# Performance work log

Measured on AMD Instinct MI355X. Metric: run time of the kernel, lower is better.

The kernel has to match this reference:

```python
import jax, jax.numpy as jnp
from jax import lax
import numpy as np

B, L, E, H, R, V = 64, 512, 256, 256, 50, 20000
NEG = 1e10  # seq_max_pool mask constant


def _conv1d(x, w, b):
    # x: (B, L, Cin) -> (B, L, Cout); kernel 3, 'same' padding (pad=1)
    y = lax.conv_general_dilated(x.transpose(0, 2, 1), w, (1,), [(1, 1)],
                                 dimension_numbers=('NCH', 'OIH', 'NCH'))
    return y.transpose(0, 2, 1) + b


def _lstm_step(x, h, c, W_ih, W_hh, b_ih, b_hh):
    # single-step LSTM, PyTorch gate order (i, f, g, o)
    gates = x @ W_ih.T + b_ih + h @ W_hh.T + b_hh
    i, f, g, o = jnp.split(gates, 4, axis=-1)
    c = jax.nn.sigmoid(f) * c + jax.nn.sigmoid(i) * jnp.tanh(g)
    h = jax.nn.sigmoid(o) * jnp.tanh(c)
    return h, c


def _attention(q, ctx, W_attn, b_attn):
    # Luong attention (IBM seq2seq style). q: (B,E), ctx: (B,L,E)
    scores = jnp.einsum('be,ble->bl', q, ctx)
    attn = jax.nn.softmax(scores, axis=-1)
    mix = jnp.einsum('bl,ble->be', attn, ctx)
    return jnp.tanh(jnp.concatenate([mix, q], axis=-1) @ W_attn.T + b_attn)


def setup_inputs() -> dict:
    key = jax.random.key(0)
    ks = jax.random.split(key, 25)
    s = 0.05
    return {
        'encoder_o': jax.random.normal(ks[0], (B, L, E), jnp.float32),
        'h0': jax.random.normal(ks[1], (B, H), jnp.float32),
        'c0': jax.random.normal(ks[2], (B, H), jnp.float32),
        'sos_emb': jax.random.normal(ks[3], (E,), jnp.float32) * s,
        'rel_emb': jax.random.normal(ks[4], (R, E), jnp.float32) * s,
        'W_ih': jax.random.normal(ks[5], (4 * H, E), jnp.float32) * s,
        'W_hh': jax.random.normal(ks[6], (4 * H, H), jnp.float32) * s,
        'b_ih': jax.random.normal(ks[7], (4 * H,), jnp.float32) * s,
        'b_hh': jax.random.normal(ks[8], (4 * H,), jnp.float32) * s,
        'W_attn': jax.random.normal(ks[9], (E, 2 * E), jnp.float32) * s,
        'b_attn': jax.random.normal(ks[10], (E,), jnp.float32) * s,
        'conv_rel_w': jax.random.normal(ks[11], (E, 2 * H, 3), jnp.float32) * s,
        'conv_rel_b': jax.random.normal(ks[12], (E,), jnp.float32) * s,
        'conv_ent_w': jax.random.normal(ks[13], (E, 2 * H, 3), jnp.float32) * s,
        'conv_ent_b': jax.random.normal(ks[14], (E,), jnp.float32) * s,
        'W_rel': jax.random.normal(ks[15], (R, E), jnp.float32) * s,
        'b_rel': jax.random.normal(ks[16], (R,), jnp.float32) * s,
        'w_e1': jax.random.normal(ks[17], (E,), jnp.float32) * s,
        'b_e1': jax.random.normal(ks[18], (1,), jnp.float32) * s,
        'w_e2': jax.random.normal(ks[19], (E,), jnp.float32) * s,
        'b_e2': jax.random.normal(ks[20], (1,), jnp.float32) * s,
        'T': jax.random.randint(ks[21], (B, L), 0, V),
        'R_in': jax.random.randint(ks[22], (B,), 0, R),
        'S_K1': jax.random.randint(ks[23], (B,), 0, L),
        'S_K2': jax.random.randint(ks[24], (B,), 0, L),
    }


def reference(encoder_o, h0, c0, sos_emb, rel_emb, W_ih, W_hh, b_ih, b_hh,
              W_attn, b_attn, conv_rel_w, conv_rel_b, conv_ent_w, conv_ent_b,
              W_rel, b_rel, w_e1, b_e1, w_e2, b_e2, T, R_in, S_K1, S_K2):
    # train_forward, order=('subject','predicate','object') -> sos2ent, ent2rel, rel2ent
    # dropout is identity (eval mode)
    mask = (T > 0).astype(encoder_o.dtype)[..., None]  # (B,L,1)
    bidx = jnp.arange(B)

    def step(inp, h, c, enc, conv_w, conv_b):
        # forward_step: one LSTM step + attention over enc
        h, c = _lstm_step(inp, h, c, W_ih, W_hh, b_ih, b_hh)
        out = _attention(h, enc, W_attn, b_attn)  # (B,E)
        # seq_and_vec + permute + conv1d + permute
        cat = jnp.concatenate([enc, jnp.broadcast_to(out[:, None, :], enc.shape)], axis=-1)
        new_enc = _conv1d(cat, conv_w, conv_b)  # (B,L,E)
        a = jax.nn.gelu(new_enc, approximate=False)
        return a, new_enc, h, c

    # step 1: sos -> entity heads
    a, enc1, h, c = step(jnp.broadcast_to(sos_emb, (B, E)), h0, c0, encoder_o,
                         conv_ent_w, conv_ent_b)
    t1e1 = a @ w_e1 + b_e1  # (B,L)
    t1e2 = a @ w_e2 + b_e2

    # step 2: gathered entity span vectors -> relation logits (masked max-pool)
    inp = enc1[bidx, S_K1] + enc1[bidx, S_K2]  # seq_gather + sum, (B,E)
    a, enc2, h, c = step(inp, h, c, enc1, conv_rel_w, conv_rel_b)
    logits = a @ W_rel.T + b_rel  # (B,L,R)
    t2rel = jnp.max(logits - (1.0 - mask) * NEG, axis=1)  # seq_max_pool -> (B,R)

    # step 3: relation embedding -> entity heads
    a, enc3, h, c = step(rel_emb[R_in], h, c, enc2, conv_ent_w, conv_ent_b)
    t3e1 = a @ w_e1 + b_e1
    t3e2 = a @ w_e2 + b_e2

    return (t1e1, t1e2, t2rel, t3e1, t3e2)
```

## Files before the change

### kernel.cpp

```cpp
#include <hip/hip_runtime.h>
#include <math.h>

#define B_ 64
#define L_ 512
#define E_ 256
#define H_ 256
#define R_ 50
#define NEG_ 1.0e10f

typedef __bf16 bf16x8 __attribute__((ext_vector_type(8)));
typedef float f32x4 __attribute__((ext_vector_type(4)));

__device__ __forceinline__ float sigmoidf_(float x) { return 1.0f / (1.0f + expf(-x)); }
__device__ __forceinline__ float geluf_(float x) { return 0.5f * x * (1.0f + erff(x * 0.7071067811865476f)); }
__device__ __forceinline__ unsigned short f2bf(float x) {
    unsigned u = __float_as_uint(x);
    return (unsigned short)((u + 0x7fffu + ((u >> 16) & 1u)) >> 16);
}
__device__ __forceinline__ float bf2f(unsigned u) { return __uint_as_float(u << 16); }

__global__ void k_tobf16(const float* __restrict__ in, unsigned short* __restrict__ out) {
    size_t idx = (size_t)blockIdx.x * 256 + threadIdx.x;
    float4 v = *(const float4*)&in[idx * 4];
    unsigned short s[4] = {f2bf(v.x), f2bf(v.y), f2bf(v.z), f2bf(v.w)};
    uint2 p;
    p.x = (unsigned)s[0] | ((unsigned)s[1] << 16);
    p.y = (unsigned)s[2] | ((unsigned)s[3] << 16);
    *(uint2*)&out[idx * 4] = p;
}

__global__ void k_packB(const float* __restrict__ w, unsigned short* __restrict__ bp) {
    int idx = blockIdx.x * 256 + threadIdx.x;
    if (idx >= 16 * 24 * 64) return;
    int l = idx & 63, kc = (idx >> 6) % 24, of = idx / (24 * 64);
    int o = of * 16 + (l & 15);
    int k = kc >> 3;
    int cb = ((kc & 7) << 5) + ((l >> 4) << 3);
    unsigned short v[8];
#pragma unroll
    for (int j = 0; j < 8; ++j) v[j] = f2bf(w[(size_t)o * 1536 + (size_t)(cb + j) * 3 + k]);
    unsigned int* dst = (unsigned int*)&bp[(size_t)idx * 8];
#pragma unroll
    for (int j = 0; j < 4; ++j) dst[j] = (unsigned int)v[2 * j] | ((unsigned int)v[2 * j + 1] << 16);
}

__global__ void k_packW(const float* __restrict__ W_rel, unsigned short* __restrict__ wp) {
    int idx = blockIdx.x * 256 + threadIdx.x;
    if (idx >= 4 * 8 * 64) return;
    int l = idx & 63, kc = (idx >> 6) & 7, of = idx / (8 * 64);
    int r = of * 16 + (l & 15);
    int k = kc * 32 + ((l >> 4) << 3);
    unsigned short v[8];
#pragma unroll
    for (int j = 0; j < 8; ++j) v[j] = (r < R_) ? f2bf(W_rel[(size_t)r * E_ + k + j]) : 0;
    unsigned int* dst = (unsigned int*)&wp[(size_t)idx * 8];
#pragma unroll
    for (int j = 0; j < 4; ++j) dst[j] = (unsigned int)v[2 * j] | ((unsigned int)v[2 * j + 1] << 16);
}

__global__ void k_packC(const float* __restrict__ w, float* __restrict__ wpk) {
    int idx = blockIdx.x * 256 + threadIdx.x;
    int o = idx >> 8, c = idx & 255;
    const float* p = &w[(size_t)o * 1536 + 768 + c * 3];
    float w0 = p[0], w1 = p[1], w2 = p[2];
    wpk[c * 256 + o] = w0;
    wpk[65536 + c * 256 + o] = w0 + w1 + w2;
    wpk[131072 + c * 256 + o] = w2;
}

__global__ void k_packWT(const float* __restrict__ W_attn, float* __restrict__ WT) {
    int idx = blockIdx.x * 256 + threadIdx.x;
    int o = idx >> 9, k = idx & 511;
    WT[k * 256 + o] = W_attn[idx];
}

template <int MODE>
__global__ __launch_bounds__(256) void k_lstm_gemm(
    const float* __restrict__ xsrc_f, const unsigned short* __restrict__ encg,
    const int* __restrict__ i1, const int* __restrict__ i2, const int* __restrict__ rin,
    const float* __restrict__ hprev,
    const float* __restrict__ W_ih, const float* __restrict__ W_hh,
    float* __restrict__ gates) {
    const int g0 = blockIdx.x * 64;
    const int half = blockIdx.y, z = blockIdx.z;
    const int t = threadIdx.x, tx = t & 15, ty = t >> 4;
    __shared__ float Xs[64][68];
    __shared__ float Wt[64][68];
    const float* Wsrc = half ? W_hh : W_ih;
    float acc[4][4] = {{0.f}};
    for (int kb = z * 128; kb < z * 128 + 128; kb += 64) {
        __syncthreads();
#pragma unroll
        for (int i = 0; i < 4; ++i) {
            int idx = i * 256 + t;
            int row = idx >> 4, kk = (idx & 15) << 2;
            float4 xv;
            if (half) {
                xv = *(const float4*)&hprev[row * 256 + kb + kk];
            } else if (MODE == 0) {
                xv = *(const float4*)&xsrc_f[kb + kk];
            } else if (MODE == 2) {
                xv = *(const float4*)&xsrc_f[(size_t)rin[row] * 256 + kb + kk];
            } else {
                const unsigned short* p1 = &encg[((size_t)row * L_ + i1[row]) * E_ + kb + kk];
                const unsigned short* p2 = &encg[((size_t)row * L_ + i2[row]) * E_ + kb + kk];
                uint2 a = *(const uint2*)p1, b2 = *(const uint2*)p2;
                xv.x = bf2f(a.x & 0xffffu) + bf2f(b2.x & 0xffffu);
                xv.y = bf2f(a.x >> 16) + bf2f(b2.x >> 16);
                xv.z = bf2f(a.y & 0xffffu) + bf2f(b2.y & 0xffffu);
                xv.w = bf2f(a.y >> 16) + bf2f(b2.y >> 16);
            }
            *(float4*)&Xs[row][kk] = xv;
            *(float4*)&Wt[row][kk] = *(const float4*)&Wsrc[(size_t)(g0 + row) * 256 + kb + kk];
        }
        __syncthreads();
#pragma unroll
        for (int kk = 0; kk < 64; kk += 4) {
            float4 xv[4], wv[4];
#pragma unroll
            for (int i = 0; i < 4; ++i) xv[i] = *(const float4*)&Xs[ty * 4 + i][kk];
#pragma unroll
            for (int j = 0; j < 4; ++j) wv[j] = *(const float4*)&Wt[tx * 4 + j][kk];
#pragma unroll
            for (int i = 0; i < 4; ++i)
#pragma unroll
                for (int j = 0; j < 4; ++j)
                    acc[i][j] += xv[i].x * wv[j].x + xv[i].y * wv[j].y + xv[i].z * wv[j].z + xv[i].w * wv[j].w;
        }
    }
    const int seg = half * 2 + z;
#pragma unroll
    for (int i = 0; i < 4; ++i)
#pragma unroll
        for (int j = 0; j < 4; ++j)
            gates[(size_t)seg * 65536 + (size_t)(ty * 4 + i) * 1024 + g0 + tx * 4 + j] = acc[i][j];
}

__global__ __launch_bounds__(256) void k_attn_part(
    const float* __restrict__ gates, const float* __restrict__ b_ih, const float* __restrict__ b_hh,
    const float* __restrict__ c_in, float* __restrict__ c_out, float* __restrict__ h_out,
    const unsigned short* __restrict__ encbf,
    float* __restrict__ mixp, float* __restrict__ stats) {
    int b = blockIdx.y, ch = blockIdx.x, t = threadIdx.x;
    __shared__ float hs[E_];
    __shared__ float scp[64][4];
    __shared__ float sc[64];
    {
        size_t ba = (size_t)b * 1024;
        float g4[4];
#pragma unroll
        for (int g = 0; g < 4; ++g) {
            float acc = b_ih[g * 256 + t] + b_hh[g * 256 + t];
#pragma unroll
            for (int seg = 0; seg < 4; ++seg) acc += gates[(size_t)seg * 65536 + ba + g * 256 + t];
            g4[g] = acc;
        }
        float c = sigmoidf_(g4[1]) * c_in[b * H_ + t] + sigmoidf_(g4[0]) * tanhf(g4[2]);
        float hv = sigmoidf_(g4[3]) * tanhf(c);
        hs[t] = hv;
        if (ch == 0) { h_out[b * H_ + t] = hv; c_out[b * H_ + t] = c; }
    }
    __syncthreads();
    {
        int row = t >> 2, es = t & 3;
        const uint4* p = (const uint4*)&encbf[((size_t)b * L_ + ch * 64 + row) * E_ + es * 64];
        float acc = 0.f;
#pragma unroll
        for (int k = 0; k < 8; ++k) {
            uint4 q = p[k];
            int e0 = es * 64 + k * 8;
            acc += bf2f(q.x & 0xffffu) * hs[e0] + bf2f(q.x >> 16) * hs[e0 + 1]
                 + bf2f(q.y & 0xffffu) * hs[e0 + 2] + bf2f(q.y >> 16) * hs[e0 + 3]
                 + bf2f(q.z & 0xffffu) * hs[e0 + 4] + bf2f(q.z >> 16) * hs[e0 + 5]
                 + bf2f(q.w & 0xffffu) * hs[e0 + 6] + bf2f(q.w >> 16) * hs[e0 + 7];
        }
        scp[row][es] = acc;
    }
    __syncthreads();
    if (t < 64) {
        float v = scp[t][0] + scp[t][1] + scp[t][2] + scp[t][3];
        float m = v;
#pragma unroll
        for (int off = 32; off; off >>= 1) m = fmaxf(m, __shfl_xor(m, off));
        float ev = expf(v - m);
        float s = ev;
#pragma unroll
        for (int off = 32; off; off >>= 1) s += __shfl_xor(s, off);
        sc[t] = ev;
        if (t == 0) {
            stats[((size_t)b * 8 + ch) * 2] = m;
            stats[((size_t)b * 8 + ch) * 2 + 1] = s;
        }
    }
    __syncthreads();
    float acc = 0.f;
    const unsigned short* base = &encbf[((size_t)b * L_ + ch * 64) * E_ + t];
#pragma unroll 8
    for (int l = 0; l < 64; ++l) acc += sc[l] * bf2f((unsigned)base[(size_t)l * E_]);
    mixp[((size_t)b * 8 + ch) * E_ + t] = acc;
}

__global__ __launch_bounds__(256) void k_post1(
    const float* __restrict__ mixp, const float* __restrict__ stats,
    const float* __restrict__ h, const float* __restrict__ WT_attn,
    const float* __restrict__ b_attn, float* __restrict__ aout) {
    int b = blockIdx.x, oc = blockIdx.y, t = threadIdx.x;
    __shared__ float cat[512];
    __shared__ float red[16][16][4];
    {
        float M = -3.0e38f;
#pragma unroll
        for (int i = 0; i < 8; ++i) M = fmaxf(M, stats[(b * 8 + i) * 2]);
        float denom = 0.f, mixv = 0.f;
#pragma unroll
        for (int i = 0; i < 8; ++i) {
            float w = expf(stats[(b * 8 + i) * 2] - M);
            denom += stats[(b * 8 + i) * 2 + 1] * w;
            mixv += mixp[((size_t)b * 8 + i) * E_ + t] * w;
        }
        cat[t] = mixv / denom;
        cat[256 + t] = h[b * H_ + t];
    }
    __syncthreads();
    int ocol = t & 15, ks = t >> 4;
    int o4 = oc * 64 + ocol * 4;
    float a0 = 0.f, a1 = 0.f, a2 = 0.f, a3 = 0.f;
    const float* wp = &WT_attn[(size_t)(ks * 32) * 256 + o4];
#pragma unroll 8
    for (int k = 0; k < 32; ++k) {
        float4 w = *(const float4*)&wp[(size_t)k * 256];
        float cv = cat[ks * 32 + k];
        a0 += cv * w.x; a1 += cv * w.y; a2 += cv * w.z; a3 += cv * w.w;
    }
    red[ks][ocol][0] = a0; red[ks][ocol][1] = a1; red[ks][ocol][2] = a2; red[ks][ocol][3] = a3;
    __syncthreads();
    if (t < 64) {
        int oc2 = t >> 2, j = t & 3;
        float s = 0.f;
#pragma unroll
        for (int k2 = 0; k2 < 16; ++k2) s += red[k2][oc2][j];
        int o = oc * 64 + t;
        aout[b * E_ + o] = tanhf(s + b_attn[o]);
    }
}

__global__ __launch_bounds__(256) void k_post2(
    const float* __restrict__ aout, const float* __restrict__ wpk,
    float* __restrict__ cr0, float* __restrict__ fullv, float* __restrict__ cr2) {
    int b = blockIdx.x, m = blockIdx.y, t = threadIdx.x;
    __shared__ float os[256];
    __shared__ float red[4][64][4];
    os[t] = aout[b * E_ + t];
    __syncthreads();
    int ocol = t & 63, cs = t >> 6;
    int o4 = ocol * 4;
    const float* wp = &wpk[(size_t)m * 65536 + (size_t)(cs * 64) * 256 + o4];
    float a0 = 0.f, a1 = 0.f, a2 = 0.f, a3 = 0.f;
#pragma unroll 8
    for (int c = 0; c < 64; ++c) {
        float4 w = *(const float4*)&wp[(size_t)c * 256];
        float v = os[cs * 64 + c];
        a0 += v * w.x; a1 += v * w.y; a2 += v * w.z; a3 += v * w.w;
    }
    red[cs][ocol][0] = a0; red[cs][ocol][1] = a1; red[cs][ocol][2] = a2; red[cs][ocol][3] = a3;
    __syncthreads();
    int oc2 = t >> 2, j = t & 3;
    float s = red[0][oc2][j] + red[1][oc2][j] + red[2][oc2][j] + red[3][oc2][j];
    float* dst = (m == 0) ? cr0 : (m == 1) ? fullv : cr2;
    dst[b * E_ + t] = s;
}

template <bool FUSE_HEADS, bool WRITE_OUT>
__global__ __launch_bounds__(256) void k_conv_mfma(
    const unsigned short* __restrict__ encbf, const unsigned short* __restrict__ bp,
    const float* __restrict__ bias, const float* __restrict__ fullv,
    const float* __restrict__ cr0, const float* __restrict__ cr2,
    unsigned short* __restrict__ enc_out,
    const float* __restrict__ w_e1, const float* __restrict__ b_e1,
    const float* __restrict__ w_e2, const float* __restrict__ b_e2,
    float* __restrict__ o1, float* __restrict__ o2) {
    const int b = blockIdx.y, l0 = blockIdx.x * 64;
    const int t = threadIdx.x, lane = t & 63, wid = t >> 6;
    __shared__ unsigned short As[66 * 256];
    __shared__ float hsum[2][4][64];

    for (int u = t; u < 66 * 32; u += 256) {
        int row = u >> 5, cu = u & 31;
        int l = l0 - 1 + row;
        uint4 v = {0u, 0u, 0u, 0u};
        if (l >= 0 && l < L_) v = *(const uint4*)&encbf[((size_t)b * L_ + l) * E_ + cu * 8];
        *(uint4*)&As[row * 256 + ((cu ^ (row & 7)) << 3)] = v;
    }
    __syncthreads();

    const int wo4 = wid * 4;
    f32x4 zero = {0.f, 0.f, 0.f, 0.f};
    f32x4 acc[4][4];
#pragma unroll
    for (int i = 0; i < 4; ++i)
#pragma unroll
        for (int j = 0; j < 4; ++j) acc[i][j] = zero;
    const int arow = lane & 15, agrp = lane >> 4;

#pragma unroll 2
    for (int kc = 0; kc < 24; ++kc) {
        const int k = kc >> 3;
        const int g = ((kc & 7) << 2) + agrp;
        bf16x8 a[4], bv[4];
#pragma unroll
        for (int mi = 0; mi < 4; ++mi) {
            int r = mi * 16 + arow + k;
            a[mi] = *(const bf16x8*)&As[r * 256 + ((g ^ (r & 7)) << 3)];
        }
#pragma unroll
        for (int ni = 0; ni < 4; ++ni)
            bv[ni] = *(const bf16x8*)&bp[(((size_t)(wo4 + ni) * 24 + kc) * 64 + lane) * 8];
#pragma unroll
        for (int mi = 0; mi < 4; ++mi)
#pragma unroll
            for (int ni = 0; ni < 4; ++ni)
                acc[mi][ni] = __builtin_amdgcn_mfma_f32_16x16x32_bf16(a[mi], bv[ni], acc[mi][ni], 0, 0, 0);
    }

    float biasv[4], c0v[4], c2v[4], we1[4], we2[4];
#pragma unroll
    for (int ni = 0; ni < 4; ++ni) {
        int o = (wo4 + ni) * 16 + (lane & 15);
        biasv[ni] = bias[o] + fullv[b * E_ + o];
        c0v[ni] = cr0[b * E_ + o];
        c2v[ni] = cr2[b * E_ + o];
        if (FUSE_HEADS) { we1[ni] = w_e1[o]; we2[ni] = w_e2[o]; }
    }
    __syncthreads();

#pragma unroll
    for (int mi = 0; mi < 4; ++mi) {
#pragma unroll
        for (int r = 0; r < 4; ++r) {
            int lloc = mi * 16 + agrp * 4 + r;
            int lrow = l0 + lloc;
            float p1 = 0.f, p2 = 0.f;
#pragma unroll
            for (int ni = 0; ni < 4; ++ni) {
                float vv = acc[mi][ni][r] + biasv[ni];
                if (lrow == 0) vv -= c0v[ni];
                if (lrow == L_ - 1) vv -= c2v[ni];
                if (WRITE_OUT) As[lloc * 256 + (wo4 + ni) * 16 + (lane & 15)] = f2bf(vv);
                if (FUSE_HEADS) {
                    float gv = geluf_(vv);
                    p1 += gv * we1[ni];
                    p2 += gv * we2[ni];
                }
            }
            if (FUSE_HEADS) {
#pragma unroll
                for (int off = 1; off < 16; off <<= 1) {
                    p1 += __shfl_xor(p1, off);
                    p2 += __shfl_xor(p2, off);
                }
                if ((lane & 15) == 0) {
                    hsum[0][wid][lloc] = p1;
                    hsum[1][wid][lloc] = p2;
                }
            }
        }
    }
    __syncthreads();
    if (WRITE_OUT) {
        for (int u = t; u < 64 * 32; u += 256) {
            int row = u >> 5, cu = u & 31;
            *(uint4*)&enc_out[((size_t)b * L_ + l0 + row) * E_ + cu * 8] = *(const uint4*)&As[row * 256 + cu * 8];
        }
    }
    if (FUSE_HEADS && t < 128) {
        int hh = t >> 6, row = t & 63;
        float s = hsum[hh][0][row] + hsum[hh][1][row] + hsum[hh][2][row] + hsum[hh][3][row];
        float* dst = hh ? o2 : o1;
        const float* bb = hh ? b_e2 : b_e1;
        dst[(size_t)b * L_ + l0 + row] = s + bb[0];
    }
}

__global__ __launch_bounds__(256) void k_relmax_mfma(
    const unsigned short* __restrict__ encbf, const unsigned short* __restrict__ wp,
    const float* __restrict__ b_rel, const int* __restrict__ T,
    float* __restrict__ pmax) {
    const int b = blockIdx.y, l0 = blockIdx.x * 64;
    const int t = threadIdx.x, lane = t & 63, wid = t >> 6;
    __shared__ unsigned short As[64 * 256];
    __shared__ int Tm[64];
    __shared__ float pm[4][64];

    if (t < 64) Tm[t] = T[b * L_ + l0 + t];
    for (int u = t; u < 64 * 32; u += 256) {
        int row = u >> 5, cu = u & 31;
        uint4 q = *(const uint4*)&encbf[((size_t)b * L_ + l0 + row) * E_ + cu * 8];
        unsigned short s[8];
        unsigned qa[4] = {q.x, q.y, q.z, q.w};
#pragma unroll
        for (int j = 0; j < 4; ++j) {
            s[2 * j] = f2bf(geluf_(bf2f(qa[j] & 0xffffu)));
            s[2 * j + 1] = f2bf(geluf_(bf2f(qa[j] >> 16)));
        }
        uint4 p;
        p.x = (unsigned)s[0] | ((unsigned)s[1] << 16);
        p.y = (unsigned)s[2] | ((unsigned)s[3] << 16);
        p.z = (unsigned)s[4] | ((unsigned)s[5] << 16);
        p.w = (unsigned)s[6] | ((unsigned)s[7] << 16);
        *(uint4*)&As[row * 256 + ((cu ^ (row & 7)) << 3)] = p;
    }
    __syncthreads();

    f32x4 zero = {0.f, 0.f, 0.f, 0.f};
    f32x4 acc[4] = {zero, zero, zero, zero};
    const int arow = wid * 16 + (lane & 15);
    const int agrp = lane >> 4;
#pragma unroll 2
    for (int kc = 0; kc < 8; ++kc) {
        int g = (kc << 2) + agrp;
        bf16x8 a0 = *(const bf16x8*)&As[arow * 256 + ((g ^ (arow & 7)) << 3)];
#pragma unroll
        for (int ni = 0; ni < 4; ++ni) {
            bf16x8 bv = *(const bf16x8*)&wp[(((size_t)ni * 8 + kc) * 64 + lane) * 8];
            acc[ni] = __builtin_amdgcn_mfma_f32_16x16x32_bf16(a0, bv, acc[ni], 0, 0, 0);
        }
    }

    const int lloc_base = wid * 16 + ((lane >> 4) << 2);
#pragma unroll
    for (int ni = 0; ni < 4; ++ni) {
        int r = ni * 16 + (lane & 15);
        float brel = (r < R_) ? b_rel[r] : 0.f;
        float v = -3.0e38f;
#pragma unroll
        for (int rg = 0; rg < 4; ++rg) {
            float logit = acc[ni][rg] + brel;
            float pen = (Tm[lloc_base + rg] > 0) ? 0.f : NEG_;
            v = fmaxf(v, logit - pen);
        }
        v = fmaxf(v, __shfl_xor(v, 16));
        v = fmaxf(v, __shfl_xor(v, 32));
        if (lane < 16) pm[wid][ni * 16 + lane] = v;
    }
    __syncthreads();
    if (t < 64) {
        float m = fmaxf(fmaxf(pm[0][t], pm[1][t]), fmaxf(pm[2][t], pm[3][t]));
        pmax[((size_t)b * 8 + blockIdx.x) * 64 + t] = m;
    }
}

__global__ void k_relmax_red(const float* __restrict__ pmax, float* __restrict__ t2rel) {
    int b = blockIdx.x, r = threadIdx.x;
    if (r >= R_) return;
    float m = -3.0e38f;
    for (int ch = 0; ch < 8; ++ch) m = fmaxf(m, pmax[((size_t)b * 8 + ch) * 64 + r]);
    t2rel[b * R_ + r] = m;
}

extern "C" void kernel_launch(void* const* d_in, const int* in_sizes, int n_in,
                              void* d_out, int out_size, void* d_ws, size_t ws_size,
                              hipStream_t stream) {
    const float* encoder_o = (const float*)d_in[0];
    const float* h0 = (const float*)d_in[1];
    const float* c0 = (const float*)d_in[2];
    const float* sos_emb = (const float*)d_in[3];
    const float* rel_emb = (const float*)d_in[4];
    const float* W_ih = (const float*)d_in[5];
    const float* W_hh = (const float*)d_in[6];
    const float* b_ih = (const float*)d_in[7];
    const float* b_hh = (const float*)d_in[8];
    const float* W_attn = (const float*)d_in[9];
    const float* b_attn = (const float*)d_in[10];
    const float* conv_rel_w = (const float*)d_in[11];
    const float* conv_rel_b = (const float*)d_in[12];
    const float* conv_ent_w = (const float*)d_in[13];
    const float* conv_ent_b = (const float*)d_in[14];
    const float* W_rel = (const float*)d_in[15];
    const float* b_rel = (const float*)d_in[16];
    const float* w_e1 = (const float*)d_in[17];
    const float* b_e1 = (const float*)d_in[18];
    const float* w_e2 = (const float*)d_in[19];
    const float* b_e2 = (const float*)d_in[20];
    const int* T = (const int*)d_in[21];
    const int* R_in = (const int*)d_in[22];
    const int* S_K1 = (const int*)d_in[23];
    const int* S_K2 = (const int*)d_in[24];

    float* out = (float*)d_out;
    float* t1e1 = out;
    float* t1e2 = out + 32768;
    float* t2rel = out + 65536;
    float* t3e1 = out + 68736;
    float* t3e2 = out + 101504;

    float* ws = (float*)d_ws;
    size_t off = 0;
    unsigned short* encBF0 = (unsigned short*)(ws + off); off += (size_t)B_ * L_ * E_ / 2;
    unsigned short* encA = (unsigned short*)(ws + off); off += (size_t)B_ * L_ * E_ / 2;
    unsigned short* encB = (unsigned short*)(ws + off); off += (size_t)B_ * L_ * E_ / 2;
    float* gates = ws + off; off += 4 * 65536;
    float* hbuf = ws + off; off += B_ * H_;
    float* cb1 = ws + off; off += B_ * H_;
    float* cb2 = ws + off; off += B_ * H_;
    float* cb3 = ws + off; off += B_ * H_;
    float* mixp = ws + off; off += (size_t)B_ * 8 * E_;
    float* stats = ws + off; off += B_ * 8 * 2;
    float* aoutb = ws + off; off += B_ * E_;
    float* fullv = ws + off; off += B_ * E_;
    float* cr0 = ws + off; off += B_ * E_;
    float* cr2 = ws + off; off += B_ * E_;
    float* pmax = ws + off; off += B_ * 8 * 64;
    float* wpkE = ws + off; off += 3 * 65536;
    float* wpkR = ws + off; off += 3 * 65536;
    float* WTat = ws + off; off += 131072;
    unsigned short* bpE = (unsigned short*)(ws + off); off += 16 * 24 * 64 * 8 / 2;
    unsigned short* bpR = (unsigned short*)(ws + off); off += 16 * 24 * 64 * 8 / 2;
    unsigned short* wpR = (unsigned short*)(ws + off); off += 4 * 8 * 64 * 8 / 2;

    dim3 convGrid(8, B_);
    dim3 attnGrid(8, B_);
    dim3 rmGrid(8, B_);
    dim3 lstmGrid(16, 2, 2);
    dim3 p1Grid(B_, 4);
    dim3 p2Grid(B_, 3);

    k_tobf16<<<(B_ * L_ * E_) / 1024, 256, 0, stream>>>(encoder_o, encBF0);
    k_packB<<<96, 256, 0, stream>>>(conv_ent_w, bpE);
    k_packB<<<96, 256, 0, stream>>>(conv_rel_w, bpR);
    k_packW<<<8, 256, 0, stream>>>(W_rel, wpR);
    k_packC<<<256, 256, 0, stream>>>(conv_ent_w, wpkE);
    k_packC<<<256, 256, 0, stream>>>(conv_rel_w, wpkR);
    k_packWT<<<512, 256, 0, stream>>>(W_attn, WTat);

    k_lstm_gemm<0><<<lstmGrid, 256, 0, stream>>>(sos_emb, nullptr, nullptr, nullptr, nullptr,
                                                 h0, W_ih, W_hh, gates);
    k_attn_part<<<attnGrid, 256, 0, stream>>>(gates, b_ih, b_hh, c0, cb1, hbuf, encBF0, mixp, stats);
    k_post1<<<p1Grid, 256, 0, stream>>>(mixp, stats, hbuf, WTat, b_attn, aoutb);
    k_post2<<<p2Grid, 256, 0, stream>>>(aoutb, wpkE, cr0, fullv, cr2);
    k_conv_mfma<true, true><<<convGrid, 256, 0, stream>>>(encBF0, bpE, conv_ent_b, fullv, cr0, cr2,
                                                          encA, w_e1, b_e1, w_e2, b_e2, t1e1, t1e2);

    k_lstm_gemm<1><<<lstmGrid, 256, 0, stream>>>(nullptr, encA, S_K1, S_K2, nullptr,
                                                 hbuf, W_ih, W_hh, gates);
    k_attn_part<<<attnGrid, 256, 0, stream>>>(gates, b_ih, b_hh, cb1, cb2, hbuf, encA, mixp, stats);
    k_post1<<<p1Grid, 256, 0, stream>>>(mixp, stats, hbuf, WTat, b_attn, aoutb);
    k_post2<<<p2Grid, 256, 0, stream>>>(aoutb, wpkR, cr0, fullv, cr2);
    k_conv_mfma<false, true><<<convGrid, 256, 0, stream>>>(encA, bpR, conv_rel_b, fullv, cr0, cr2,
                                                           encB, nullptr, nullptr, nullptr, nullptr,
                                                           nullptr, nullptr);
    k_relmax_mfma<<<rmGrid, 256, 0, stream>>>(encB, wpR, b_rel, T, pmax);
    k_relmax_red<<<B_, 64, 0, stream>>>(pmax, t2rel);

    k_lstm_gemm<2><<<lstmGrid, 256, 0, stream>>>(rel_emb, nullptr, nullptr, nullptr, R_in,
                                                 hbuf, W_ih, W_hh, gates);
    k_attn_part<<<attnGrid, 256, 0, stream>>>(gates, b_ih, b_hh, cb2, cb3, hbuf, encB, mixp, stats);
    k_post1<<<p1Grid, 256, 0, stream>>>(mixp, stats, hbuf, WTat, b_attn, aoutb);
    k_post2<<<p2Grid, 256, 0, stream>>>(aoutb, wpkE, cr0, fullv, cr2);
    k_conv_mfma<true, false><<<convGrid, 256, 0, stream>>>(encB, bpE, conv_ent_b, fullv, cr0, cr2,
                                                           nullptr, w_e1, b_e1, w_e2, b_e2, t3e1, t3e2);
}
```

Measured before the change: 227.4 us.

## Merge pack kernels into one launch and split conv MFMA across eight waves

The seven preprocessing kernels (bf16 conversion of the encoder output and the weight packs) become one kernel that dispatches on block index, which removes launch overhead. The conv MFMA kernel now runs 512 threads per block with eight waves, each owning two output column tiles instead of four. It also software-prefetches the B fragments for the next k-chunk and reduces the head partial sums over eight waves. Per-wave work and register pressure go down and more waves can hide latency. In exchange, each A fragment loaded from LDS is reused across fewer MFMAs, so LDS read traffic per MFMA goes up.

Result: faster. 190.5 us (-16.2%).

```diff
diff --git a/kernel.cpp b/kernel.cpp
--- a/kernel.cpp
+++ b/kernel.cpp
@@ -19,59 +19,60 @@
 }
 __device__ __forceinline__ float bf2f(unsigned u) { return __uint_as_float(u << 16); }
 
-__global__ void k_tobf16(const float* __restrict__ in, unsigned short* __restrict__ out) {
-    size_t idx = (size_t)blockIdx.x * 256 + threadIdx.x;
-    float4 v = *(const float4*)&in[idx * 4];
-    unsigned short s[4] = {f2bf(v.x), f2bf(v.y), f2bf(v.z), f2bf(v.w)};
-    uint2 p;
-    p.x = (unsigned)s[0] | ((unsigned)s[1] << 16);
-    p.y = (unsigned)s[2] | ((unsigned)s[3] << 16);
-    *(uint2*)&out[idx * 4] = p;
-}
-
-__global__ void k_packB(const float* __restrict__ w, unsigned short* __restrict__ bp) {
-    int idx = blockIdx.x * 256 + threadIdx.x;
-    if (idx >= 16 * 24 * 64) return;
-    int l = idx & 63, kc = (idx >> 6) % 24, of = idx / (24 * 64);
-    int o = of * 16 + (l & 15);
-    int k = kc >> 3;
-    int cb = ((kc & 7) << 5) + ((l >> 4) << 3);
-    unsigned short v[8];
-#pragma unroll
-    for (int j = 0; j < 8; ++j) v[j] = f2bf(w[(size_t)o * 1536 + (size_t)(cb + j) * 3 + k]);
-    unsigned int* dst = (unsigned int*)&bp[(size_t)idx * 8];
-#pragma unroll
-    for (int j = 0; j < 4; ++j) dst[j] = (unsigned int)v[2 * j] | ((unsigned int)v[2 * j + 1] << 16);
-}
-
-__global__ void k_packW(const float* __restrict__ W_rel, unsigned short* __restrict__ wp) {
-    int idx = blockIdx.x * 256 + threadIdx.x;
-    if (idx >= 4 * 8 * 64) return;
-    int l = idx & 63, kc = (idx >> 6) & 7, of = idx / (8 * 64);
-    int r = of * 16 + (l & 15);
-    int k = kc * 32 + ((l >> 4) << 3);
-    unsigned short v[8];
-#pragma unroll
-    for (int j = 0; j < 8; ++j) v[j] = (r < R_) ? f2bf(W_rel[(size_t)r * E_ + k + j]) : 0;
-    unsigned int* dst = (unsigned int*)&wp[(size_t)idx * 8];
-#pragma unroll
-    for (int j = 0; j < 4; ++j) dst[j] = (unsigned int)v[2 * j] | ((unsigned int)v[2 * j + 1] << 16);
-}
-
-__global__ void k_packC(const float* __restrict__ w, float* __restrict__ wpk) {
-    int idx = blockIdx.x * 256 + threadIdx.x;
-    int o = idx >> 8, c = idx & 255;
-    const float* p = &w[(size_t)o * 1536 + 768 + c * 3];
-    float w0 = p[0], w1 = p[1], w2 = p[2];
-    wpk[c * 256 + o] = w0;
-    wpk[65536 + c * 256 + o] = w0 + w1 + w2;
-    wpk[131072 + c * 256 + o] = w2;
-}
-
-__global__ void k_packWT(const float* __restrict__ W_attn, float* __restrict__ WT) {
-    int idx = blockIdx.x * 256 + threadIdx.x;
-    int o = idx >> 9, k = idx & 511;
-    WT[k * 256 + o] = W_attn[idx];
+__global__ void k_packs(const float* __restrict__ encoder_o, unsigned short* __restrict__ encBF0,
+                        const float* __restrict__ conv_ent_w, const float* __restrict__ conv_rel_w,
+                        unsigned short* __restrict__ bpE, unsigned short* __restrict__ bpR,
+                        const float* __restrict__ W_rel, unsigned short* __restrict__ wpR,
+                        float* __restrict__ wpkE, float* __restrict__ wpkR,
+                        const float* __restrict__ W_attn, float* __restrict__ WTat) {
+    const int blk = blockIdx.x, t = threadIdx.x;
+    if (blk < 8192) {
+        size_t idx = (size_t)blk * 256 + t;
+        float4 v = *(const float4*)&encoder_o[idx * 4];
+        uint2 p;
+        p.x = (unsigned)f2bf(v.x) | ((unsigned)f2bf(v.y) << 16);
+        p.y = (unsigned)f2bf(v.z) | ((unsigned)f2bf(v.w) << 16);
+        *(uint2*)&encBF0[idx * 4] = p;
+    } else if (blk < 8384) {
+        const float* w = (blk < 8288) ? conv_ent_w : conv_rel_w;
+        unsigned short* bp = (blk < 8288) ? bpE : bpR;
+        int idx = (blk - ((blk < 8288) ? 8192 : 8288)) * 256 + t;
+        int l = idx & 63, kc = (idx >> 6) % 24, of = idx / (24 * 64);
+        int o = of * 16 + (l & 15);
+        int k = kc >> 3;
+        int cb = ((kc & 7) << 5) + ((l >> 4) << 3);
+        unsigned short v[8];
+#pragma unroll
+        for (int j = 0; j < 8; ++j) v[j] = f2bf(w[(size_t)o * 1536 + (size_t)(cb + j) * 3 + k]);
+        unsigned int* dst = (unsigned int*)&bp[(size_t)idx * 8];
+#pragma unroll
+        for (int j = 0; j < 4; ++j) dst[j] = (unsigned int)v[2 * j] | ((unsigned int)v[2 * j + 1] << 16);
+    } else if (blk < 8392) {
+        int idx = (blk - 8384) * 256 + t;
+        int l = idx & 63, kc = (idx >> 6) & 7, of = idx / (8 * 64);
+        int r = of * 16 + (l & 15);
+        int k = kc * 32 + ((l >> 4) << 3);
+        unsigned short v[8];
+#pragma unroll
+        for (int j = 0; j < 8; ++j) v[j] = (r < R_) ? f2bf(W_rel[(size_t)r * E_ + k + j]) : 0;
+        unsigned int* dst = (unsigned int*)&wpR[(size_t)idx * 8];
+#pragma unroll
+        for (int j = 0; j < 4; ++j) dst[j] = (unsigned int)v[2 * j] | ((unsigned int)v[2 * j + 1] << 16);
+    } else if (blk < 8904) {
+        const float* w = (blk < 8648) ? conv_ent_w : conv_rel_w;
+        float* wpk = (blk < 8648) ? wpkE : wpkR;
+        int idx = (blk - ((blk < 8648) ? 8392 : 8648)) * 256 + t;
+        int o = idx >> 8, c = idx & 255;
+        const float* p = &w[(size_t)o * 1536 + 768 + c * 3];
+        float w0 = p[0], w1 = p[1], w2 = p[2];
+        wpk[c * 256 + o] = w0;
+        wpk[65536 + c * 256 + o] = w0 + w1 + w2;
+        wpk[131072 + c * 256 + o] = w2;
+    } else {
+        int idx = (blk - 8904) * 256 + t;
+        int o = idx >> 9, k = idx & 511;
+        WTat[k * 256 + o] = W_attn[idx];
+    }
 }
 
 template <int MODE>
@@ -271,7 +272,7 @@
 }
 
 template <bool FUSE_HEADS, bool WRITE_OUT>
-__global__ __launch_bounds__(256) void k_conv_mfma(
+__global__ __launch_bounds__(512, 4) void k_conv_mfma(
     const unsigned short* __restrict__ encbf, const unsigned short* __restrict__ bp,
     const float* __restrict__ bias, const float* __restrict__ fullv,
     const float* __restrict__ cr0, const float* __restrict__ cr2,
@@ -282,9 +283,9 @@
     const int b = blockIdx.y, l0 = blockIdx.x * 64;
     const int t = threadIdx.x, lane = t & 63, wid = t >> 6;
     __shared__ unsigned short As[66 * 256];
-    __shared__ float hsum[2][4][64];
-
-    for (int u = t; u < 66 * 32; u += 256) {
+    __shared__ float hsum[2][8][64];
+
+    for (int u = t; u < 66 * 32; u += 512) {
         int row = u >> 5, cu = u & 31;
         int l = l0 - 1 + row;
         uint4 v = {0u, 0u, 0u, 0u};
@@ -293,43 +294,47 @@
     }
     __syncthreads();
 
-    const int wo4 = wid * 4;
+    const int wo2 = wid * 2;
     f32x4 zero = {0.f, 0.f, 0.f, 0.f};
-    f32x4 acc[4][4];
-#pragma unroll
-    for (int i = 0; i < 4; ++i)
-#pragma unroll
-        for (int j = 0; j < 4; ++j) acc[i][j] = zero;
+    f32x4 acc[4][2];
+#pragma unroll
+    for (int i = 0; i < 4; ++i) { acc[i][0] = zero; acc[i][1] = zero; }
     const int arow = lane & 15, agrp = lane >> 4;
-
-#pragma unroll 2
+    const unsigned short* bp0 = &bp[((size_t)wo2 * 24 * 64 + lane) * 8];
+    const unsigned short* bp1 = &bp[((size_t)(wo2 + 1) * 24 * 64 + lane) * 8];
+
+    bf16x8 bn0 = *(const bf16x8*)bp0;
+    bf16x8 bn1 = *(const bf16x8*)bp1;
+#pragma unroll 4
     for (int kc = 0; kc < 24; ++kc) {
+        bf16x8 b0 = bn0, b1 = bn1;
+        if (kc < 23) {
+            bn0 = *(const bf16x8*)&bp0[(size_t)(kc + 1) * 512];
+            bn1 = *(const bf16x8*)&bp1[(size_t)(kc + 1) * 512];
+        }
         const int k = kc >> 3;
         const int g = ((kc & 7) << 2) + agrp;
-        bf16x8 a[4], bv[4];
+        bf16x8 a[4];
 #pragma unroll
         for (int mi = 0; mi < 4; ++mi) {
             int r = mi * 16 + arow + k;
             a[mi] = *(const bf16x8*)&As[r * 256 + ((g ^ (r & 7)) << 3)];
         }
 #pragma unroll
-        for (int ni = 0; ni < 4; ++ni)
-            bv[ni] = *(const bf16x8*)&bp[(((size_t)(wo4 + ni) * 24 + kc) * 64 + lane) * 8];
-#pragma unroll
-        for (int mi = 0; mi < 4; ++mi)
-#pragma unroll
-            for (int ni = 0; ni < 4; ++ni)
-                acc[mi][ni] = __builtin_amdgcn_mfma_f32_16x16x32_bf16(a[mi], bv[ni], acc[mi][ni], 0, 0, 0);
-    }
-
-    float biasv[4], c0v[4], c2v[4], we1[4], we2[4];
-#pragma unroll
-    for (int ni = 0; ni < 4; ++ni) {
-        int o = (wo4 + ni) * 16 + (lane & 15);
+        for (int mi = 0; mi < 4; ++mi) {
+            acc[mi][0] = __builtin_amdgcn_mfma_f32_16x16x32_bf16(a[mi], b0, acc[mi][0], 0, 0, 0);
+            acc[mi][1] = __builtin_amdgcn_mfma_f32_16x16x32_bf16(a[mi], b1, acc[mi][1], 0, 0, 0);
+        }
+    }
+
+    float biasv[2], c0v[2], c2v[2], we1v[2], we2v[2];
+#pragma unroll
+    for (int ni = 0; ni < 2; ++ni) {
+        int o = (wo2 + ni) * 16 + (lane & 15);
         biasv[ni] = bias[o] + fullv[b * E_ + o];
         c0v[ni] = cr0[b * E_ + o];
         c2v[ni] = cr2[b * E_ + o];
-        if (FUSE_HEADS) { we1[ni] = w_e1[o]; we2[ni] = w_e2[o]; }
+        if (FUSE_HEADS) { we1v[ni] = w_e1[o]; we2v[ni] = w_e2[o]; }
     }
     __syncthreads();
 
@@ -341,15 +346,15 @@
             int lrow = l0 + lloc;
             float p1 = 0.f, p2 = 0.f;
 #pragma unroll
-            for (int ni = 0; ni < 4; ++ni) {
+            for (int ni = 0; ni < 2; ++ni) {
                 float vv = acc[mi][ni][r] + biasv[ni];
                 if (lrow == 0) vv -= c0v[ni];
                 if (lrow == L_ - 1) vv -= c2v[ni];
-                if (WRITE_OUT) As[lloc * 256 + (wo4 + ni) * 16 + (lane & 15)] = f2bf(vv);
+                if (WRITE_OUT) As[lloc * 256 + (wo2 + ni) * 16 + (lane & 15)] = f2bf(vv);
                 if (FUSE_HEADS) {
                     float gv = geluf_(vv);
-                    p1 += gv * we1[ni];
-                    p2 += gv * we2[ni];
+                    p1 += gv * we1v[ni];
+                    p2 += gv * we2v[ni];
                 }
             }
             if (FUSE_HEADS) {
@@ -367,14 +372,16 @@
     }
     __syncthreads();
     if (WRITE_OUT) {
-        for (int u = t; u < 64 * 32; u += 256) {
+        for (int u = t; u < 64 * 32; u += 512) {
             int row = u >> 5, cu = u & 31;
             *(uint4*)&enc_out[((size_t)b * L_ + l0 + row) * E_ + cu * 8] = *(const uint4*)&As[row * 256 + cu * 8];
         }
     }
     if (FUSE_HEADS && t < 128) {
         int hh = t >> 6, row = t & 63;
-        float s = hsum[hh][0][row] + hsum[hh][1][row] + hsum[hh][2][row] + hsum[hh][3][row];
+        float s = 0.f;
+#pragma unroll
+        for (int w = 0; w < 8; ++w) s += hsum[hh][w][row];
         float* dst = hh ? o2 : o1;
         const float* bb = hh ? b_e2 : b_e1;
         dst[(size_t)b * L_ + l0 + row] = s + bb[0];
@@ -524,20 +531,15 @@
     dim3 p1Grid(B_, 4);
     dim3 p2Grid(B_, 3);
 
-    k_tobf16<<<(B_ * L_ * E_) / 1024, 256, 0, stream>>>(encoder_o, encBF0);
-    k_packB<<<96, 256, 0, stream>>>(conv_ent_w, bpE);
-    k_packB<<<96, 256, 0, stream>>>(conv_rel_w, bpR);
-    k_packW<<<8, 256, 0, stream>>>(W_rel, wpR);
-    k_packC<<<256, 256, 0, stream>>>(conv_ent_w, wpkE);
-    k_packC<<<256, 256, 0, stream>>>(conv_rel_w, wpkR);
-    k_packWT<<<512, 256, 0, stream>>>(W_attn, WTat);
+    k_packs<<<9416, 256, 0, stream>>>(encoder_o, encBF0, conv_ent_w, conv_rel_w,
+                                      bpE, bpR, W_rel, wpR, wpkE, wpkR, W_attn, WTat);
 
     k_lstm_gemm<0><<<lstmGrid, 256, 0, stream>>>(sos_emb, nullptr, nullptr, nullptr, nullptr,
                                                  h0, W_ih, W_hh, gates);
     k_attn_part<<<attnGrid, 256, 0, stream>>>(gates, b_ih, b_hh, c0, cb1, hbuf, encBF0, mixp, stats);
     k_post1<<<p1Grid, 256, 0, stream>>>(mixp, stats, hbuf, WTat, b_attn, aoutb);
     k_post2<<<p2Grid, 256, 0, stream>>>(aoutb, wpkE, cr0, fullv, cr2);
-    k_conv_mfma<true, true><<<convGrid, 256, 0, stream>>>(encBF0, bpE, conv_ent_b, fullv, cr0, cr2,
+    k_conv_mfma<true, true><<<convGrid, 512, 0, stream>>>(encBF0, bpE, conv_ent_b, fullv, cr0, cr2,
                                                           encA, w_e1, b_e1, w_e2, b_e2, t1e1, t1e2);
 
     k_lstm_gemm<1><<<lstmGrid, 256, 0, stream>>>(nullptr, encA, S_K1, S_K2, nullptr,
@@ -545,7 +547,7 @@
     k_attn_part<<<attnGrid, 256, 0, stream>>>(gates, b_ih, b_hh, cb1, cb2, hbuf, encA, mixp, stats);
     k_post1<<<p1Grid, 256, 0, stream>>>(mixp, stats, hbuf, WTat, b_attn, aoutb);
     k_post2<<<p2Grid, 256, 0, stream>>>(aoutb, wpkR, cr0, fullv, cr2);
-    k_conv_mfma<false, true><<<convGrid, 256, 0, stream>>>(encA, bpR, conv_rel_b, fullv, cr0, cr2,
+    k_conv_mfma<false, true><<<convGrid, 512, 0, stream>>>(encA, bpR, conv_rel_b, fullv, cr0, cr2,
                                                            encB, nullptr, nullptr, nullptr, nullptr,
                                                            nullptr, nullptr);
     k_relmax_mfma<<<rmGrid, 256, 0, stream>>>(encB, wpR, b_rel, T, pmax);
@@ -556,6 +558,6 @@
     k_attn_part<<<attnGrid, 256, 0, stream>>>(gates, b_ih, b_hh, cb2, cb3, hbuf, encB, mixp, stats);
     k_post1<<<p1Grid, 256, 0, stream>>>(mixp, stats, hbuf, WTat, b_attn, aoutb);
     k_post2<<<p2Grid, 256, 0, stream>>>(aoutb, wpkE, cr0, fullv, cr2);
-    k_conv_mfma<true, false><<<convGrid, 256, 0, stream>>>(encB, bpE, conv_ent_b, fullv, cr0, cr2,
+    k_conv_mfma<true, false><<<convGrid, 512, 0, stream>>>(encB, bpE, conv_ent_b, fullv, cr0, cr2,
                                                            nullptr, w_e1, b_e1, w_e2, b_e2, t3e1, t3e2);
 }
```
